# Kernel optimization log

Measured on AMD Instinct MI355X. Metric: run time of the kernel, lower is better.

Reference implementation:

```python
import jax, jax.numpy as jnp
import numpy as np

B, C, D = 16, 512, 256
K = 16        # spatio_topk
RD = 128      # rec_dim
H = 8         # num_heads
FFN = 1024    # temporal_ffn
TEMP = 0.5    # temperature


def setup_inputs() -> dict:
    key = jax.random.key(0)
    ks = jax.random.split(key, 8)
    s = lambda k, shape: (jax.random.normal(k, shape, jnp.float32) * 0.02)
    return dict(
        x=jax.random.normal(ks[0], (B, C, D), jnp.float32),
        wq_rec=s(ks[1], (RD, D)),
        wk_rec=s(ks[2], (RD, D)),
        in_proj_w=s(ks[3], (3 * D, D)),
        in_proj_b=jnp.zeros((3 * D,), jnp.float32),
        out_w=s(ks[4], (D, D)),
        out_b=jnp.zeros((D,), jnp.float32),
        ln1_g=jnp.ones((D,), jnp.float32),
        ln1_b=jnp.zeros((D,), jnp.float32),
        mlp_w1=s(ks[5], (FFN, D)),
        mlp_b1=jnp.zeros((FFN,), jnp.float32),
        mlp_w2=s(ks[6], (D, FFN)),
        mlp_b2=jnp.zeros((D,), jnp.float32),
        ln2_g=jnp.ones((D,), jnp.float32),
        ln2_b=jnp.zeros((D,), jnp.float32),
    )


def _ln(x, g, b, eps=1e-5):
    m = x.mean(-1, keepdims=True)
    v = ((x - m) ** 2).mean(-1, keepdims=True)
    return (x - m) * jax.lax.rsqrt(v + eps) * g + b


def reference(x, wq_rec, wk_rec, in_proj_w, in_proj_b, out_w, out_b,
              ln1_g, ln1_b, mlp_w1, mlp_b1, mlp_w2, mlp_b2, ln2_g, ln2_b):
    b, c, d = x.shape
    # --- ST_Rec_Module (training branch: straight-through top-k routing) ---
    xq = x @ wq_rec.T                                   # (B,C,RD)
    xk = x @ wk_rec.T
    logits = jnp.einsum('bqd,bkd->bqk', xq, xk) / TEMP  # (B,C,C)
    idx = jax.lax.top_k(logits, K)[1]                   # (B,C,K)
    z_hard = jax.nn.one_hot(idx, c, dtype=x.dtype)      # (B,C,K,C)
    # cumulative mask of previously-selected channels (exclusive cumsum)
    prev = jnp.cumsum(z_hard, axis=2)
    prev = jnp.concatenate([jnp.zeros_like(prev[:, :, :1]), prev[:, :, :-1]], axis=2)
    mask = prev > 0
    zs = jnp.where(mask, -1e30, logits[:, :, None, :] / TEMP)  # logits/temp twice, as in source
    z_soft = jax.nn.softmax(zs, axis=-1)
    z = z_hard + z_soft - jax.lax.stop_gradient(z_soft)        # straight-through
    rec_x = jnp.einsum('bqkc,bcd->bqkd', z, x)                 # (B,C,K,D)

    # --- ST_Channel_Module: per-channel cross-attention, query length 1 ---
    hd = d // H
    wq, wk, wv = in_proj_w[:d], in_proj_w[d:2 * d], in_proj_w[2 * d:]
    bq, bk, bv = in_proj_b[:d], in_proj_b[d:2 * d], in_proj_b[2 * d:]
    q = (x @ wq.T + bq).reshape(b, c, H, hd)                   # (B,C,H,hd)
    k = (rec_x @ wk.T + bk).reshape(b, c, K, H, hd)
    v = (rec_x @ wv.T + bv).reshape(b, c, K, H, hd)
    scores = jnp.einsum('bchd,bckhd->bchk', q, k) / np.float32(np.sqrt(hd))
    attn = jax.nn.softmax(scores, axis=-1)
    ctx = jnp.einsum('bchk,bckhd->bchd', attn, v).reshape(b, c, d)
    attn_out = ctx @ out_w.T + out_b
    x1 = _ln(attn_out + x, ln1_g, ln1_b)

    # --- ST_Temporal_Module (Identity projections, gelu FFN + LN) ---
    h = jax.nn.gelu(x1 @ mlp_w1.T + mlp_b1, approximate=False)
    h = h @ mlp_w2.T + mlp_b2
    x2 = _ln(h + x1, ln2_g, ln2_b)
    return x2
```

## Files before the change

kernel.cpp:

```cpp
#include <hip/hip_runtime.h>
#include <hip/hip_bf16.h>
#include <math.h>

#define B_   16
#define C_   512
#define D_   256
#define K_   16
#define RD_  128
#define H_   8
#define HD_  32
#define FFN_ 1024
#define M_   (B_ * C_)

typedef __attribute__((ext_vector_type(8))) short bf16x8;
typedef __attribute__((ext_vector_type(4))) float f32x4;

typedef __attribute__((address_space(1))) const int ga_int;
typedef __attribute__((address_space(3))) int ls_int;

static __device__ __forceinline__ short f2bf(float v) {
    __hip_bfloat16 h = __float2bfloat16(v);
    return *(short*)&h;
}
static __device__ __forceinline__ float bf2f(short s) {
    __hip_bfloat16 h = *(__hip_bfloat16*)&s;
    return __bfloat162float(h);
}

#define N8_X    (M_ * D_ / 8)
#define N8_INW  (768 * D_ / 8)
#define N8_OUTW (D_ * D_ / 8)
#define N8_W1   (FFN_ * D_ / 8)
#define N8_W2   (D_ * FFN_ / 8)
#define N8_WQ   (RD_ * D_ / 8)
#define N8_ALL  (N8_X + N8_INW + N8_OUTW + N8_W1 + N8_W2 + 2 * N8_WQ)

__global__ __launch_bounds__(256) void convert_all_kernel(
    const float* __restrict__ x, const float* __restrict__ inw,
    const float* __restrict__ outw, const float* __restrict__ w1,
    const float* __restrict__ w2, const float* __restrict__ wq,
    const float* __restrict__ wk,
    short* __restrict__ xbf, short* __restrict__ xlo,
    short* __restrict__ inwbf, short* __restrict__ outwbf,
    short* __restrict__ w1bf, short* __restrict__ w2bf,
    short* __restrict__ wqh, short* __restrict__ wql,
    short* __restrict__ wkh, short* __restrict__ wkl)
{
    int i = blockIdx.x * 256 + threadIdx.x;
    if (i >= N8_ALL) return;

    const float* s; short* dh; short* dl = nullptr; int off;
    if      (i < N8_X)                    { s = x;    dh = xbf;    dl = xlo; off = i; }
    else if (i < N8_X + N8_INW)           { s = inw;  dh = inwbf;  off = i - N8_X; }
    else if (i < N8_X + N8_INW + N8_OUTW) { s = outw; dh = outwbf; off = i - N8_X - N8_INW; }
    else if (i < N8_X + N8_INW + N8_OUTW + N8_W1)
                                          { s = w1;   dh = w1bf;   off = i - N8_X - N8_INW - N8_OUTW; }
    else if (i < N8_X + N8_INW + N8_OUTW + N8_W1 + N8_W2)
                                          { s = w2;   dh = w2bf;   off = i - N8_X - N8_INW - N8_OUTW - N8_W1; }
    else if (i < N8_X + N8_INW + N8_OUTW + N8_W1 + N8_W2 + N8_WQ)
                                          { s = wq;   dh = wqh; dl = wql; off = i - N8_X - N8_INW - N8_OUTW - N8_W1 - N8_W2; }
    else                                  { s = wk;   dh = wkh; dl = wkl; off = i - N8_X - N8_INW - N8_OUTW - N8_W1 - N8_W2 - N8_WQ; }

    const float4* sp = (const float4*)s + (size_t)off * 2;
    float4 v0 = sp[0], v1 = sp[1];
    float f[8] = {v0.x, v0.y, v0.z, v0.w, v1.x, v1.y, v1.z, v1.w};
    short rh[8], rl[8];
    #pragma unroll
    for (int j = 0; j < 8; ++j) {
        rh[j] = f2bf(f[j]);
        rl[j] = f2bf(f[j] - bf2f(rh[j]));
    }
    *(bf16x8*)(dh + (size_t)off * 8) = *(bf16x8*)rh;
    if (dl) *(bf16x8*)(dl + (size_t)off * 8) = *(bf16x8*)rl;
}

template<int BM, int BN, int OUT_BF16, int ACT>
__global__ __launch_bounds__(256) void gemm_mfma(
    const short* __restrict__ A, const short* __restrict__ W,
    const float* __restrict__ bias, void* __restrict__ Cout,
    int M, int N, int Kd)
{
    __shared__ short As[2][BM * 32];
    __shared__ short Bs[2][BN * 32];
    const int tid  = threadIdx.x;
    const int wave = tid >> 6;
    const int lane = tid & 63;
    const int bm = blockIdx.y * BM;
    const int bn = blockIdx.x * BN;
    constexpr int MI = BM / 32;
    constexpr int NJ = BN / 32;
    const int wr = (wave >> 1) * (BM / 2);
    const int wc = (wave & 1) * (BN / 2);

    const int fr = lane & 15;
    const int fk = (lane >> 4) * 8;

    const int r0 = tid >> 2, ch = (tid & 3) * 8;

    f32x4 acc[MI][NJ];
    #pragma unroll
    for (int i = 0; i < MI; ++i)
        #pragma unroll
        for (int j = 0; j < NJ; ++j)
            acc[i][j] = (f32x4){0.f, 0.f, 0.f, 0.f};

    auto stage = [&](int buf, int k0) {
        #pragma unroll
        for (int i = 0; i < BM / 64; ++i)
            __builtin_amdgcn_global_load_lds(
                (ga_int*)&A[(size_t)(bm + r0 + i * 64) * Kd + k0 + ch],
                (ls_int*)&As[buf][(tid + i * 256) * 8], 16, 0, 0);
        #pragma unroll
        for (int j = 0; j < BN / 64; ++j)
            __builtin_amdgcn_global_load_lds(
                (ga_int*)&W[(size_t)(bn + r0 + j * 64) * Kd + k0 + ch],
                (ls_int*)&Bs[buf][(tid + j * 256) * 8], 16, 0, 0);
    };

    stage(0, 0);
    int cur = 0;

    for (int k0 = 0; k0 < Kd; k0 += 32) {
        __syncthreads();
        if (k0 + 32 < Kd) stage(cur ^ 1, k0 + 32);

        bf16x8 af[MI], bfr[NJ];
        #pragma unroll
        for (int i = 0; i < MI; ++i) af[i]  = *(bf16x8*)&As[cur][(wr + i * 16 + fr) * 32 + fk];
        #pragma unroll
        for (int j = 0; j < NJ; ++j) bfr[j] = *(bf16x8*)&Bs[cur][(wc + j * 16 + fr) * 32 + fk];
        #pragma unroll
        for (int i = 0; i < MI; ++i)
            #pragma unroll
            for (int j = 0; j < NJ; ++j)
                acc[i][j] = __builtin_amdgcn_mfma_f32_16x16x32_bf16(af[i], bfr[j], acc[i][j], 0, 0, 0);
        cur ^= 1;
    }

    const int rowbase = (lane >> 4) * 4;
    #pragma unroll
    for (int i = 0; i < MI; ++i) {
        #pragma unroll
        for (int j = 0; j < NJ; ++j) {
            const int n = bn + wc + j * 16 + fr;
            const float bn_v = bias ? bias[n] : 0.f;
            #pragma unroll
            for (int r = 0; r < 4; ++r) {
                const int m = bm + wr + i * 16 + rowbase + r;
                float v = acc[i][j][r] + bn_v;
                if (ACT) v = 0.5f * v * (1.0f + erff(v * 0.70710678118654752f));
                if (OUT_BF16) ((short*)Cout)[(size_t)m * N + n] = f2bf(v);
                else          ((float*)Cout)[(size_t)m * N + n] = v;
            }
        }
    }
}

__global__ __launch_bounds__(256) void xqk_mfma(
    const short* __restrict__ xh, const short* __restrict__ xl,
    const short* __restrict__ wqh, const short* __restrict__ wql,
    const short* __restrict__ wkh, const short* __restrict__ wkl,
    short* __restrict__ qh, short* __restrict__ ql,
    short* __restrict__ kh, short* __restrict__ kl)
{
    __shared__ short Ah[64 * 32], Al[64 * 32], Bh[64 * 32], Bl[64 * 32];
    const short* Wh = blockIdx.z ? wkh : wqh;
    const short* Wl = blockIdx.z ? wkl : wql;
    short* Oh       = blockIdx.z ? kh : qh;
    short* Ol       = blockIdx.z ? kl : ql;

    const int tid  = threadIdx.x;
    const int wave = tid >> 6;
    const int lane = tid & 63;
    const int bm = blockIdx.y * 64;
    const int bn = blockIdx.x * 64;
    const int wr = (wave >> 1) * 32;
    const int wc = (wave & 1) * 32;
    const int fr = lane & 15;
    const int fk = (lane >> 4) * 8;
    const int r0 = tid >> 2, ch = (tid & 3) * 8;

    f32x4 acc[2][2];
    #pragma unroll
    for (int i = 0; i < 2; ++i)
        #pragma unroll
        for (int j = 0; j < 2; ++j)
            acc[i][j] = (f32x4){0.f, 0.f, 0.f, 0.f};

    for (int k0 = 0; k0 < D_; k0 += 32) {
        __builtin_amdgcn_global_load_lds((ga_int*)&xh[(size_t)(bm + r0) * D_ + k0 + ch], (ls_int*)&Ah[tid * 8], 16, 0, 0);
        __builtin_amdgcn_global_load_lds((ga_int*)&xl[(size_t)(bm + r0) * D_ + k0 + ch], (ls_int*)&Al[tid * 8], 16, 0, 0);
        __builtin_amdgcn_global_load_lds((ga_int*)&Wh[(size_t)(bn + r0) * D_ + k0 + ch], (ls_int*)&Bh[tid * 8], 16, 0, 0);
        __builtin_amdgcn_global_load_lds((ga_int*)&Wl[(size_t)(bn + r0) * D_ + k0 + ch], (ls_int*)&Bl[tid * 8], 16, 0, 0);
        __syncthreads();

        bf16x8 ah[2], al[2], bh[2], bl[2];
        #pragma unroll
        for (int i = 0; i < 2; ++i) {
            ah[i] = *(bf16x8*)&Ah[(wr + i * 16 + fr) * 32 + fk];
            al[i] = *(bf16x8*)&Al[(wr + i * 16 + fr) * 32 + fk];
        }
        #pragma unroll
        for (int j = 0; j < 2; ++j) {
            bh[j] = *(bf16x8*)&Bh[(wc + j * 16 + fr) * 32 + fk];
            bl[j] = *(bf16x8*)&Bl[(wc + j * 16 + fr) * 32 + fk];
        }
        #pragma unroll
        for (int i = 0; i < 2; ++i)
            #pragma unroll
            for (int j = 0; j < 2; ++j) {
                acc[i][j] = __builtin_amdgcn_mfma_f32_16x16x32_bf16(ah[i], bh[j], acc[i][j], 0, 0, 0);
                acc[i][j] = __builtin_amdgcn_mfma_f32_16x16x32_bf16(ah[i], bl[j], acc[i][j], 0, 0, 0);
                acc[i][j] = __builtin_amdgcn_mfma_f32_16x16x32_bf16(al[i], bh[j], acc[i][j], 0, 0, 0);
            }
        __syncthreads();
    }

    const int rowbase = (lane >> 4) * 4;
    #pragma unroll
    for (int i = 0; i < 2; ++i)
        #pragma unroll
        for (int j = 0; j < 2; ++j) {
            const int n = bn + wc + j * 16 + fr;
            #pragma unroll
            for (int r = 0; r < 4; ++r) {
                const int m = bm + wr + i * 16 + rowbase + r;
                float v = acc[i][j][r];
                short h = f2bf(v);
                Oh[(size_t)m * RD_ + n] = h;
                Ol[(size_t)m * RD_ + n] = f2bf(v - bf2f(h));
            }
        }
}

__global__ __launch_bounds__(256) void logits_mfma(
    const short* __restrict__ qh, const short* __restrict__ ql,
    const short* __restrict__ kh, const short* __restrict__ kl,
    float* __restrict__ out)
{
    __shared__ short Ah[64 * 32], Al[64 * 32], Bh[64 * 32], Bl[64 * 32];
    const int tid  = threadIdx.x;
    const int wave = tid >> 6;
    const int lane = tid & 63;
    const int base = blockIdx.z * C_;
    const int bm = blockIdx.y * 64;
    const int bn = blockIdx.x * 64;
    const int wr = (wave >> 1) * 32;
    const int wc = (wave & 1) * 32;
    const int fr = lane & 15;
    const int fk = (lane >> 4) * 8;
    const int r0 = tid >> 2, ch = (tid & 3) * 8;

    f32x4 acc[2][2];
    #pragma unroll
    for (int i = 0; i < 2; ++i)
        #pragma unroll
        for (int j = 0; j < 2; ++j)
            acc[i][j] = (f32x4){0.f, 0.f, 0.f, 0.f};

    for (int k0 = 0; k0 < RD_; k0 += 32) {
        __builtin_amdgcn_global_load_lds((ga_int*)&qh[(size_t)(base + bm + r0) * RD_ + k0 + ch], (ls_int*)&Ah[tid * 8], 16, 0, 0);
        __builtin_amdgcn_global_load_lds((ga_int*)&ql[(size_t)(base + bm + r0) * RD_ + k0 + ch], (ls_int*)&Al[tid * 8], 16, 0, 0);
        __builtin_amdgcn_global_load_lds((ga_int*)&kh[(size_t)(base + bn + r0) * RD_ + k0 + ch], (ls_int*)&Bh[tid * 8], 16, 0, 0);
        __builtin_amdgcn_global_load_lds((ga_int*)&kl[(size_t)(base + bn + r0) * RD_ + k0 + ch], (ls_int*)&Bl[tid * 8], 16, 0, 0);
        __syncthreads();

        bf16x8 ah[2], al[2], bh[2], bl[2];
        #pragma unroll
        for (int i = 0; i < 2; ++i) {
            ah[i] = *(bf16x8*)&Ah[(wr + i * 16 + fr) * 32 + fk];
            al[i] = *(bf16x8*)&Al[(wr + i * 16 + fr) * 32 + fk];
        }
        #pragma unroll
        for (int j = 0; j < 2; ++j) {
            bh[j] = *(bf16x8*)&Bh[(wc + j * 16 + fr) * 32 + fk];
            bl[j] = *(bf16x8*)&Bl[(wc + j * 16 + fr) * 32 + fk];
        }
        #pragma unroll
        for (int i = 0; i < 2; ++i)
            #pragma unroll
            for (int j = 0; j < 2; ++j) {
                acc[i][j] = __builtin_amdgcn_mfma_f32_16x16x32_bf16(ah[i], bh[j], acc[i][j], 0, 0, 0);
                acc[i][j] = __builtin_amdgcn_mfma_f32_16x16x32_bf16(ah[i], bl[j], acc[i][j], 0, 0, 0);
                acc[i][j] = __builtin_amdgcn_mfma_f32_16x16x32_bf16(al[i], bh[j], acc[i][j], 0, 0, 0);
            }
        __syncthreads();
    }

    const int rowbase = (lane >> 4) * 4;
    #pragma unroll
    for (int i = 0; i < 2; ++i)
        #pragma unroll
        for (int j = 0; j < 2; ++j) {
            const int n = bn + wc + j * 16 + fr;
            #pragma unroll
            for (int r = 0; r < 4; ++r) {
                const int m = base + bm + wr + i * 16 + rowbase + r;
                out[(size_t)m * C_ + n] = acc[i][j][r];
            }
        }
}

__global__ __launch_bounds__(256) void topk_attn_kernel(
    const float* __restrict__ logits, const float* __restrict__ qkv,
    short* __restrict__ ctxbf)
{
    const int wave = threadIdx.x >> 6;
    const int lane = threadIdx.x & 63;
    const int row  = blockIdx.x * 4 + wave;
    const int bbase = row & ~(C_ - 1);

    const float* lrow = logits + (size_t)row * C_;
    unsigned long long key[8];
    #pragma unroll
    for (int j = 0; j < 8; ++j) {
        int pos = lane * 8 + j;
        unsigned u = __float_as_uint(lrow[pos]);
        u = (u & 0x80000000u) ? ~u : (u | 0x80000000u);
        key[j] = (((unsigned long long)u) << 9) | (unsigned)(511 - pos);
    }

    int ii[K_];
    #pragma unroll
    for (int sel = 0; sel < K_; ++sel) {
        unsigned long long best = key[0];
        #pragma unroll
        for (int j = 1; j < 8; ++j) best = key[j] > best ? key[j] : best;
        #pragma unroll
        for (int s = 1; s < 64; s <<= 1) {
            unsigned long long o = __shfl_xor(best, s, 64);
            best = o > best ? o : best;
        }
        int pos = 511 - (int)(best & 511ull);
        ii[sel] = pos;
        if ((pos >> 3) == lane) key[pos & 7] = 0ull;
    }

    const float* qrow = qkv + (size_t)row * 768;
    float4 qv = *(const float4*)(qrow + lane * 4);

    float s[K_];
    #pragma unroll
    for (int k = 0; k < K_; ++k) {
        const float* kr = qkv + (size_t)(bbase + ii[k]) * 768 + 256;
        float4 kv = *(const float4*)(kr + lane * 4);
        float p = qv.x * kv.x + qv.y * kv.y + qv.z * kv.z + qv.w * kv.w;
        p += __shfl_xor(p, 1, 64);
        p += __shfl_xor(p, 2, 64);
        p += __shfl_xor(p, 4, 64);
        s[k] = p * 0.17677669529663687f;
    }

    float m = s[0];
    #pragma unroll
    for (int k = 1; k < K_; ++k) m = fmaxf(m, s[k]);
    float ssum = 0.f;
    #pragma unroll
    for (int k = 0; k < K_; ++k) { s[k] = __expf(s[k] - m); ssum += s[k]; }
    const float inv = 1.f / ssum;

    float4 acc = {0.f, 0.f, 0.f, 0.f};
    #pragma unroll
    for (int k = 0; k < K_; ++k) {
        const float* vr = qkv + (size_t)(bbase + ii[k]) * 768 + 512;
        float4 vv = *(const float4*)(vr + lane * 4);
        float w = s[k] * inv;
        acc.x += w * vv.x; acc.y += w * vv.y; acc.z += w * vv.z; acc.w += w * vv.w;
    }

    unsigned lo = (unsigned)(unsigned short)f2bf(acc.x) | ((unsigned)(unsigned short)f2bf(acc.y) << 16);
    unsigned hi = (unsigned)(unsigned short)f2bf(acc.z) | ((unsigned)(unsigned short)f2bf(acc.w) << 16);
    uint2 pk = {lo, hi};
    *(uint2*)(ctxbf + (size_t)row * D_ + lane * 4) = pk;
}

template<int WBF>
__global__ __launch_bounds__(256) void add_ln_wave_kernel(
    const float* __restrict__ a, const float* __restrict__ res,
    const float* __restrict__ g, const float* __restrict__ beta,
    float* __restrict__ out, short* __restrict__ outbf)
{
    const int wave = threadIdx.x >> 6;
    const int lane = threadIdx.x & 63;
    const int row  = blockIdx.x * 4 + wave;

    float4 va = *(const float4*)(a   + (size_t)row * D_ + lane * 4);
    float4 vr = *(const float4*)(res + (size_t)row * D_ + lane * 4);
    float4 v = {va.x + vr.x, va.y + vr.y, va.z + vr.z, va.w + vr.w};

    float t = v.x + v.y + v.z + v.w;
    #pragma unroll
    for (int s = 1; s < 64; s <<= 1) t += __shfl_xor(t, s, 64);
    const float mean = t * (1.0f / D_);

    float4 dv = {v.x - mean, v.y - mean, v.z - mean, v.w - mean};
    float sq = dv.x * dv.x + dv.y * dv.y + dv.z * dv.z + dv.w * dv.w;
    #pragma unroll
    for (int s = 1; s < 64; s <<= 1) sq += __shfl_xor(sq, s, 64);
    const float rstd = rsqrtf(sq * (1.0f / D_) + 1e-5f);

    float4 gv = *(const float4*)(g    + lane * 4);
    float4 bv = *(const float4*)(beta + lane * 4);
    float4 o = {dv.x * rstd * gv.x + bv.x, dv.y * rstd * gv.y + bv.y,
                dv.z * rstd * gv.z + bv.z, dv.w * rstd * gv.w + bv.w};
    *(float4*)(out + (size_t)row * D_ + lane * 4) = o;
    if (WBF) {
        unsigned lo = (unsigned)(unsigned short)f2bf(o.x) | ((unsigned)(unsigned short)f2bf(o.y) << 16);
        unsigned hi = (unsigned)(unsigned short)f2bf(o.z) | ((unsigned)(unsigned short)f2bf(o.w) << 16);
        uint2 pk = {lo, hi};
        *(uint2*)(outbf + (size_t)row * D_ + lane * 4) = pk;
    }
}

extern "C" void kernel_launch(void* const* d_in, const int* in_sizes, int n_in,
                              void* d_out, int out_size, void* d_ws, size_t ws_size,
                              hipStream_t stream)
{
    const float* x      = (const float*)d_in[0];
    const float* wq_rec = (const float*)d_in[1];
    const float* wk_rec = (const float*)d_in[2];
    const float* in_w   = (const float*)d_in[3];
    const float* in_b   = (const float*)d_in[4];
    const float* out_w  = (const float*)d_in[5];
    const float* out_b  = (const float*)d_in[6];
    const float* ln1_g  = (const float*)d_in[7];
    const float* ln1_b  = (const float*)d_in[8];
    const float* w1     = (const float*)d_in[9];
    const float* b1     = (const float*)d_in[10];
    const float* w2     = (const float*)d_in[11];
    const float* b2     = (const float*)d_in[12];
    const float* ln2_g  = (const float*)d_in[13];
    const float* ln2_b  = (const float*)d_in[14];
    float* out = (float*)d_out;

    float* ws = (float*)d_ws;
    float* qkv   = ws;
    short* qh    = (short*)(qkv + (size_t)M_ * 768);
    short* ql    = qh + (size_t)M_ * RD_;
    short* kh    = ql + (size_t)M_ * RD_;
    short* kl    = kh + (size_t)M_ * RD_;
    float* x1    = (float*)(kl + (size_t)M_ * RD_);
    float* ao    = x1 + (size_t)M_ * D_;
    float* U     = ao + (size_t)M_ * D_;
    float* logits = U;
    short* ctxbf  = (short*)U;
    short* x1bf   = (short*)U + (size_t)M_ * D_;
    short* hbf    = (short*)U + (size_t)2 * M_ * D_;
    float* afterU = U + (size_t)3 * M_ * D_;
    short* xbf    = (short*)afterU;
    short* xlo    = xbf   + (size_t)M_ * D_;
    short* inwbf  = xlo   + (size_t)M_ * D_;
    short* outwbf = inwbf + (size_t)768 * D_;
    short* w1bf   = outwbf + (size_t)D_ * D_;
    short* w2bf   = w1bf  + (size_t)FFN_ * D_;
    short* wqh    = w2bf  + (size_t)D_ * FFN_;
    short* wql    = wqh + (size_t)RD_ * D_;
    short* wkh    = wql + (size_t)RD_ * D_;
    short* wkl    = wkh + (size_t)RD_ * D_;

    dim3 blk(256);

    convert_all_kernel<<<dim3((N8_ALL + 255) / 256), blk, 0, stream>>>(
        x, in_w, out_w, w1, w2, wq_rec, wk_rec,
        xbf, xlo, inwbf, outwbf, w1bf, w2bf, wqh, wql, wkh, wkl);

    gemm_mfma<64, 128, 0, 0><<<dim3(768 / 128, M_ / 64), blk, 0, stream>>>(xbf, inwbf, in_b, qkv, M_, 768, D_);
    xqk_mfma<<<dim3(RD_ / 64, M_ / 64, 2), blk, 0, stream>>>(
        xbf, xlo, wqh, wql, wkh, wkl, qh, ql, kh, kl);
    logits_mfma<<<dim3(C_ / 64, C_ / 64, B_), blk, 0, stream>>>(qh, ql, kh, kl, logits);
    topk_attn_kernel<<<dim3(M_ / 4), blk, 0, stream>>>(logits, qkv, ctxbf);
    gemm_mfma<64, 64, 0, 0><<<dim3(D_ / 64, M_ / 64), blk, 0, stream>>>(ctxbf, outwbf, out_b, ao, M_, D_, D_);
    add_ln_wave_kernel<1><<<dim3(M_ / 4), blk, 0, stream>>>(ao, x, ln1_g, ln1_b, x1, x1bf);
    gemm_mfma<128, 128, 1, 1><<<dim3(FFN_ / 128, M_ / 128), blk, 0, stream>>>(x1bf, w1bf, b1, hbf, M_, FFN_, D_);
    gemm_mfma<64, 64, 0, 0><<<dim3(D_ / 64, M_ / 64), blk, 0, stream>>>(hbf, w2bf, b2, ao, M_, D_, FFN_);
    add_ln_wave_kernel<0><<<dim3(M_ / 4), blk, 0, stream>>>(ao, x1, ln2_g, ln2_b, out, nullptr);
}
```

Before: 123.9 us.

## Fuse residual add and LayerNorm into output GEMMs; store QKV in bf16

Adds a gemm_ln_mfma kernel that computes a 32-row by full-256-column tile, then adds bias and residual and applies LayerNorm in the epilogue using cross-wave partial sums in shared memory. This replaces the out-projection GEMM plus add_ln and the FFN2 GEMM plus add_ln, so the intermediate fp32 buffer is no longer written and reread and two launches go away. It also writes the QKV projection as bf16, which halves the gathered K/V traffic in the top-k attention kernel at some precision cost. Variance is now computed as E[x^2]-mean^2, and the 32-row tiles give only 256 blocks with a 1024-deep K loop for FFN2, which may underfill the GPU.

```diff
diff --git a/kernel.cpp b/kernel.cpp
--- a/kernel.cpp
+++ b/kernel.cpp
@@ -25,6 +25,15 @@
 static __device__ __forceinline__ float bf2f(short s) {
     __hip_bfloat16 h = *(__hip_bfloat16*)&s;
     return __bfloat162float(h);
+}
+static __device__ __forceinline__ float4 ld4bf(const short* p) {
+    uint2 u = *(const uint2*)p;
+    float4 r;
+    r.x = __uint_as_float((u.x & 0xffffu) << 16);
+    r.y = __uint_as_float(u.x & 0xffff0000u);
+    r.z = __uint_as_float((u.y & 0xffffu) << 16);
+    r.w = __uint_as_float(u.y & 0xffff0000u);
+    return r;
 }
 
 #define N8_X    (M_ * D_ / 8)
@@ -94,7 +103,6 @@
 
     const int fr = lane & 15;
     const int fk = (lane >> 4) * 8;
-
     const int r0 = tid >> 2, ch = (tid & 3) * 8;
 
     f32x4 acc[MI][NJ];
@@ -154,6 +162,132 @@
             }
         }
     }
+}
+
+template<int KD, int WBF>
+__global__ __launch_bounds__(256) void gemm_ln_mfma(
+    const short* __restrict__ A, const short* __restrict__ W,
+    const float* __restrict__ bias, const float* __restrict__ res,
+    const float* __restrict__ g, const float* __restrict__ beta,
+    float* __restrict__ out, short* __restrict__ outbf)
+{
+    __shared__ short As[2][32 * 32];
+    __shared__ short Bs[2][256 * 32];
+    __shared__ float part[4][32][2];
+
+    const int tid  = threadIdx.x;
+    const int wave = tid >> 6;
+    const int lane = tid & 63;
+    const int bm = blockIdx.x * 32;
+    const int wc = wave * 64;
+    const int fr = lane & 15;
+    const int fk = (lane >> 4) * 8;
+    const int r0 = tid >> 2, ch = (tid & 3) * 8;
+
+    f32x4 acc[2][4];
+    #pragma unroll
+    for (int i = 0; i < 2; ++i)
+        #pragma unroll
+        for (int j = 0; j < 4; ++j)
+            acc[i][j] = (f32x4){0.f, 0.f, 0.f, 0.f};
+
+    auto stage = [&](int buf, int k0) {
+        if (tid < 128)
+            __builtin_amdgcn_global_load_lds(
+                (ga_int*)&A[(size_t)(bm + r0) * KD + k0 + ch],
+                (ls_int*)&As[buf][tid * 8], 16, 0, 0);
+        #pragma unroll
+        for (int j = 0; j < 4; ++j)
+            __builtin_amdgcn_global_load_lds(
+                (ga_int*)&W[(size_t)(r0 + j * 64) * KD + k0 + ch],
+                (ls_int*)&Bs[buf][(tid + j * 256) * 8], 16, 0, 0);
+    };
+
+    stage(0, 0);
+    int cur = 0;
+
+    for (int k0 = 0; k0 < KD; k0 += 32) {
+        __syncthreads();
+        if (k0 + 32 < KD) stage(cur ^ 1, k0 + 32);
+
+        bf16x8 af[2], bfr[4];
+        #pragma unroll
+        for (int i = 0; i < 2; ++i) af[i]  = *(bf16x8*)&As[cur][(i * 16 + fr) * 32 + fk];
+        #pragma unroll
+        for (int j = 0; j < 4; ++j) bfr[j] = *(bf16x8*)&Bs[cur][(wc + j * 16 + fr) * 32 + fk];
+        #pragma unroll
+        for (int i = 0; i < 2; ++i)
+            #pragma unroll
+            for (int j = 0; j < 4; ++j)
+                acc[i][j] = __builtin_amdgcn_mfma_f32_16x16x32_bf16(af[i], bfr[j], acc[i][j], 0, 0, 0);
+        cur ^= 1;
+    }
+
+    const int rowbase = (lane >> 4) * 4;
+    float vv[2][4][4];
+    float sum[2][4], sq[2][4];
+    #pragma unroll
+    for (int i = 0; i < 2; ++i)
+        #pragma unroll
+        for (int r = 0; r < 4; ++r) { sum[i][r] = 0.f; sq[i][r] = 0.f; }
+
+    #pragma unroll
+    for (int i = 0; i < 2; ++i)
+        #pragma unroll
+        for (int j = 0; j < 4; ++j) {
+            const int n = wc + j * 16 + fr;
+            const float bv = bias[n];
+            #pragma unroll
+            for (int r = 0; r < 4; ++r) {
+                const int m = bm + i * 16 + rowbase + r;
+                float v = acc[i][j][r] + bv + res[(size_t)m * D_ + n];
+                vv[i][j][r] = v;
+                sum[i][r] += v;
+                sq[i][r]  += v * v;
+            }
+        }
+
+    #pragma unroll
+    for (int i = 0; i < 2; ++i)
+        #pragma unroll
+        for (int r = 0; r < 4; ++r)
+            #pragma unroll
+            for (int s = 1; s < 16; s <<= 1) {
+                sum[i][r] += __shfl_xor(sum[i][r], s, 64);
+                sq[i][r]  += __shfl_xor(sq[i][r],  s, 64);
+            }
+
+    if (fr == 0) {
+        #pragma unroll
+        for (int i = 0; i < 2; ++i)
+            #pragma unroll
+            for (int r = 0; r < 4; ++r) {
+                int ml = i * 16 + rowbase + r;
+                part[wave][ml][0] = sum[i][r];
+                part[wave][ml][1] = sq[i][r];
+            }
+    }
+    __syncthreads();
+
+    #pragma unroll
+    for (int i = 0; i < 2; ++i)
+        #pragma unroll
+        for (int r = 0; r < 4; ++r) {
+            const int ml = i * 16 + rowbase + r;
+            const float S = part[0][ml][0] + part[1][ml][0] + part[2][ml][0] + part[3][ml][0];
+            const float Q = part[0][ml][1] + part[1][ml][1] + part[2][ml][1] + part[3][ml][1];
+            const float mean = S * (1.0f / D_);
+            const float var  = Q * (1.0f / D_) - mean * mean;
+            const float rstd = rsqrtf(var + 1e-5f);
+            const int m = bm + ml;
+            #pragma unroll
+            for (int j = 0; j < 4; ++j) {
+                const int n = wc + j * 16 + fr;
+                float o = (vv[i][j][r] - mean) * rstd * g[n] + beta[n];
+                out[(size_t)m * D_ + n] = o;
+                if (WBF) outbf[(size_t)m * D_ + n] = f2bf(o);
+            }
+        }
 }
 
 __global__ __launch_bounds__(256) void xqk_mfma(
@@ -302,7 +436,7 @@
 }
 
 __global__ __launch_bounds__(256) void topk_attn_kernel(
-    const float* __restrict__ logits, const float* __restrict__ qkv,
+    const float* __restrict__ logits, const short* __restrict__ qkv,
     short* __restrict__ ctxbf)
 {
     const int wave = threadIdx.x >> 6;
@@ -336,14 +470,13 @@
         if ((pos >> 3) == lane) key[pos & 7] = 0ull;
     }
 
-    const float* qrow = qkv + (size_t)row * 768;
-    float4 qv = *(const float4*)(qrow + lane * 4);
+    const short* qrow = qkv + (size_t)row * 768;
+    float4 qv = ld4bf(qrow + lane * 4);
 
     float s[K_];
     #pragma unroll
     for (int k = 0; k < K_; ++k) {
-        const float* kr = qkv + (size_t)(bbase + ii[k]) * 768 + 256;
-        float4 kv = *(const float4*)(kr + lane * 4);
+        float4 kv = ld4bf(qkv + (size_t)(bbase + ii[k]) * 768 + 256 + lane * 4);
         float p = qv.x * kv.x + qv.y * kv.y + qv.z * kv.z + qv.w * kv.w;
         p += __shfl_xor(p, 1, 64);
         p += __shfl_xor(p, 2, 64);
@@ -362,54 +495,15 @@
     float4 acc = {0.f, 0.f, 0.f, 0.f};
     #pragma unroll
     for (int k = 0; k < K_; ++k) {
-        const float* vr = qkv + (size_t)(bbase + ii[k]) * 768 + 512;
-        float4 vv = *(const float4*)(vr + lane * 4);
+        float4 vvv = ld4bf(qkv + (size_t)(bbase + ii[k]) * 768 + 512 + lane * 4);
         float w = s[k] * inv;
-        acc.x += w * vv.x; acc.y += w * vv.y; acc.z += w * vv.z; acc.w += w * vv.w;
+        acc.x += w * vvv.x; acc.y += w * vvv.y; acc.z += w * vvv.z; acc.w += w * vvv.w;
     }
 
     unsigned lo = (unsigned)(unsigned short)f2bf(acc.x) | ((unsigned)(unsigned short)f2bf(acc.y) << 16);
     unsigned hi = (unsigned)(unsigned short)f2bf(acc.z) | ((unsigned)(unsigned short)f2bf(acc.w) << 16);
     uint2 pk = {lo, hi};
     *(uint2*)(ctxbf + (size_t)row * D_ + lane * 4) = pk;
-}
-
-template<int WBF>
-__global__ __launch_bounds__(256) void add_ln_wave_kernel(
-    const float* __restrict__ a, const float* __restrict__ res,
-    const float* __restrict__ g, const float* __restrict__ beta,
-    float* __restrict__ out, short* __restrict__ outbf)
-{
-    const int wave = threadIdx.x >> 6;
-    const int lane = threadIdx.x & 63;
-    const int row  = blockIdx.x * 4 + wave;
-
-    float4 va = *(const float4*)(a   + (size_t)row * D_ + lane * 4);
-    float4 vr = *(const float4*)(res + (size_t)row * D_ + lane * 4);
-    float4 v = {va.x + vr.x, va.y + vr.y, va.z + vr.z, va.w + vr.w};
-
-    float t = v.x + v.y + v.z + v.w;
-    #pragma unroll
-    for (int s = 1; s < 64; s <<= 1) t += __shfl_xor(t, s, 64);
-    const float mean = t * (1.0f / D_);
-
-    float4 dv = {v.x - mean, v.y - mean, v.z - mean, v.w - mean};
-    float sq = dv.x * dv.x + dv.y * dv.y + dv.z * dv.z + dv.w * dv.w;
-    #pragma unroll
-    for (int s = 1; s < 64; s <<= 1) sq += __shfl_xor(sq, s, 64);
-    const float rstd = rsqrtf(sq * (1.0f / D_) + 1e-5f);
-
-    float4 gv = *(const float4*)(g    + lane * 4);
-    float4 bv = *(const float4*)(beta + lane * 4);
-    float4 o = {dv.x * rstd * gv.x + bv.x, dv.y * rstd * gv.y + bv.y,
-                dv.z * rstd * gv.z + bv.z, dv.w * rstd * gv.w + bv.w};
-    *(float4*)(out + (size_t)row * D_ + lane * 4) = o;
-    if (WBF) {
-        unsigned lo = (unsigned)(unsigned short)f2bf(o.x) | ((unsigned)(unsigned short)f2bf(o.y) << 16);
-        unsigned hi = (unsigned)(unsigned short)f2bf(o.z) | ((unsigned)(unsigned short)f2bf(o.w) << 16);
-        uint2 pk = {lo, hi};
-        *(uint2*)(outbf + (size_t)row * D_ + lane * 4) = pk;
-    }
 }
 
 extern "C" void kernel_launch(void* const* d_in, const int* in_sizes, int n_in,
@@ -433,21 +527,18 @@
     const float* ln2_b  = (const float*)d_in[14];
     float* out = (float*)d_out;
 
-    float* ws = (float*)d_ws;
-    float* qkv   = ws;
-    short* qh    = (short*)(qkv + (size_t)M_ * 768);
+    short* qkvbf = (short*)d_ws;
+    short* qh    = qkvbf + (size_t)M_ * 768;
     short* ql    = qh + (size_t)M_ * RD_;
     short* kh    = ql + (size_t)M_ * RD_;
     short* kl    = kh + (size_t)M_ * RD_;
     float* x1    = (float*)(kl + (size_t)M_ * RD_);
-    float* ao    = x1 + (size_t)M_ * D_;
-    float* U     = ao + (size_t)M_ * D_;
+    float* U     = x1 + (size_t)M_ * D_;
     float* logits = U;
-    short* ctxbf  = (short*)U;
-    short* x1bf   = (short*)U + (size_t)M_ * D_;
-    short* hbf    = (short*)U + (size_t)2 * M_ * D_;
-    float* afterU = U + (size_t)3 * M_ * D_;
-    short* xbf    = (short*)afterU;
+    short* ctxbf  = (short*)(U + (size_t)M_ * 512);
+    short* x1bf   = ctxbf + (size_t)M_ * D_;
+    short* hbf    = x1bf  + (size_t)M_ * D_;
+    short* xbf    = hbf   + (size_t)M_ * FFN_;
     short* xlo    = xbf   + (size_t)M_ * D_;
     short* inwbf  = xlo   + (size_t)M_ * D_;
     short* outwbf = inwbf + (size_t)768 * D_;
@@ -464,14 +555,14 @@
         x, in_w, out_w, w1, w2, wq_rec, wk_rec,
         xbf, xlo, inwbf, outwbf, w1bf, w2bf, wqh, wql, wkh, wkl);
 
-    gemm_mfma<64, 128, 0, 0><<<dim3(768 / 128, M_ / 64), blk, 0, stream>>>(xbf, inwbf, in_b, qkv, M_, 768, D_);
+    gemm_mfma<64, 128, 1, 0><<<dim3(768 / 128, M_ / 64), blk, 0, stream>>>(xbf, inwbf, in_b, qkvbf, M_, 768, D_);
     xqk_mfma<<<dim3(RD_ / 64, M_ / 64, 2), blk, 0, stream>>>(
         xbf, xlo, wqh, wql, wkh, wkl, qh, ql, kh, kl);
     logits_mfma<<<dim3(C_ / 64, C_ / 64, B_), blk, 0, stream>>>(qh, ql, kh, kl, logits);
-    topk_attn_kernel<<<dim3(M_ / 4), blk, 0, stream>>>(logits, qkv, ctxbf);
-    gemm_mfma<64, 64, 0, 0><<<dim3(D_ / 64, M_ / 64), blk, 0, stream>>>(ctxbf, outwbf, out_b, ao, M_, D_, D_);
-    add_ln_wave_kernel<1><<<dim3(M_ / 4), blk, 0, stream>>>(ao, x, ln1_g, ln1_b, x1, x1bf);
+    topk_attn_kernel<<<dim3(M_ / 4), blk, 0, stream>>>(logits, qkvbf, ctxbf);
+    gemm_ln_mfma<256, 1><<<dim3(M_ / 32), blk, 0, stream>>>(
+        ctxbf, outwbf, out_b, x, ln1_g, ln1_b, x1, x1bf);
     gemm_mfma<128, 128, 1, 1><<<dim3(FFN_ / 128, M_ / 128), blk, 0, stream>>>(x1bf, w1bf, b1, hbf, M_, FFN_, D_);
-    gemm_mfma<64, 64, 0, 0><<<dim3(D_ / 64, M_ / 64), blk, 0, stream>>>(hbf, w2bf, b2, ao, M_, D_, FFN_);
-    add_ln_wave_kernel<0><<<dim3(M_ / 4), blk, 0, stream>>>(ao, x1, ln2_g, ln2_b, out, nullptr);
-}
+    gemm_ln_mfma<1024, 0><<<dim3(M_ / 32), blk, 0, stream>>>(
+        hbf, w2bf, b2, x1, ln2_g, ln2_b, out, nullptr);
+}
```

Result: no change. 123.1 us (-0.6%).
